# Performance work log

Hardware: AMD Instinct MI355X
Metric: run time of the kernel (lower is better)

## Reference

```python
import jax, jax.numpy as jnp
import numpy as np

B, H, W, DIM = 8, 32, 32, 768
NUM_HEADS = 12
HEAD_DIM = DIM // NUM_HEADS  # 64
SCALE = HEAD_DIM ** (-0.5)


def setup_inputs() -> dict:
    key = jax.random.key(0)
    ks = jax.random.split(key, 7)
    return {
        "x": jax.random.normal(ks[0], (B, H, W, DIM), dtype=jnp.float32),
        "qkv_w": jax.random.normal(ks[1], (DIM, 3 * DIM), dtype=jnp.float32) * 0.02,
        "qkv_b": jax.random.normal(ks[2], (3 * DIM,), dtype=jnp.float32) * 0.02,
        "proj_w": jax.random.normal(ks[3], (DIM, DIM), dtype=jnp.float32) * 0.02,
        "proj_b": jax.random.normal(ks[4], (DIM,), dtype=jnp.float32) * 0.02,
        "rel_pos_h": jax.random.normal(ks[5], (2 * H - 1, HEAD_DIM), dtype=jnp.float32) * 0.02,
        "rel_pos_w": jax.random.normal(ks[6], (2 * W - 1, HEAD_DIM), dtype=jnp.float32) * 0.02,
    }


def _get_rel_pos(q_size, k_size, rel_pos):
    # q_size == k_size here, so no interpolation branch; coords in [0, 2*size-2]
    coords = jnp.arange(q_size)[:, None] - jnp.arange(k_size)[None, :] + (k_size - 1)
    return rel_pos[coords]  # [q_size, k_size, head_dim]


def reference(x, qkv_w, qkv_b, proj_w, proj_b, rel_pos_h, rel_pos_w):
    b, h, w, dim = x.shape
    n = h * w
    qkv = x.reshape(b, n, dim) @ qkv_w + qkv_b                      # [B, N, 3*dim]
    qkv = qkv.reshape(b, n, 3, NUM_HEADS, HEAD_DIM)
    qkv = jnp.transpose(qkv, (2, 0, 3, 1, 4)).reshape(3, b * NUM_HEADS, n, HEAD_DIM)
    q, k, v = qkv[0], qkv[1], qkv[2]                                # [B*nh, N, hd]

    attn = jnp.einsum("bqc,bkc->bqk", q * SCALE, k)                 # [B*nh, N, N]

    Rh = _get_rel_pos(h, h, rel_pos_h)                              # [H, H, hd]
    Rw = _get_rel_pos(w, w, rel_pos_w)                              # [W, W, hd]
    r_q = q.reshape(b * NUM_HEADS, h, w, HEAD_DIM)
    rel_h = jnp.einsum("bhwc,hkc->bhwk", r_q, Rh)                   # [B*nh, H, W, H]
    rel_w = jnp.einsum("bhwc,wkc->bhwk", r_q, Rw)                   # [B*nh, H, W, W]
    attn = (attn.reshape(b * NUM_HEADS, h, w, h, w)
            + rel_h[:, :, :, :, None]
            + rel_w[:, :, :, None, :]).reshape(b * NUM_HEADS, n, n)

    attn = jax.nn.softmax(attn, axis=-1)
    out = jnp.einsum("bqk,bkc->bqc", attn, v)                       # [B*nh, N, hd]
    out = out.reshape(b, NUM_HEADS, h, w, HEAD_DIM)
    out = jnp.transpose(out, (0, 2, 3, 1, 4)).reshape(b, h, w, dim)
    return out @ proj_w + proj_b
```

## Files before the change

### kernel.cpp

```cpp
#include <hip/hip_runtime.h>


typedef __bf16 bf16;
typedef __bf16 bf16x8 __attribute__((ext_vector_type(8)));
typedef __bf16 bf16x4 __attribute__((ext_vector_type(4)));
typedef __bf16 bf16x2 __attribute__((ext_vector_type(2)));
typedef float f32x4 __attribute__((ext_vector_type(4)));
typedef unsigned int u32x2 __attribute__((ext_vector_type(2)));

#define MFMA16(a, b, c) __builtin_amdgcn_mfma_f32_16x16x32_bf16((a), (b), (c), 0, 0, 0)

__device__ __forceinline__ void gld_lds16(const void* g, void* l) {
  __builtin_amdgcn_global_load_lds(
      (const __attribute__((address_space(1))) void*)g,
      (__attribute__((address_space(3))) void*)l, 16, 0, 0);
}

__global__ __launch_bounds__(256) void prep_k(const float* __restrict__ x,
                                              const float* __restrict__ qkv_w,
                                              const float* __restrict__ proj_w,
                                              const float* __restrict__ rh,
                                              const float* __restrict__ rw,
                                              bf16* __restrict__ xb,
                                              bf16* __restrict__ WqkvT,
                                              bf16* __restrict__ WprojT,
                                              bf16* __restrict__ rhb,
                                              bf16* __restrict__ rwb) {
  __shared__ float tile[64][65];
  int b = blockIdx.x, tid = threadIdx.x;
  if (b >= 616) {
    int i = (b - 616) * 256 + tid;
    float4 a = ((const float4*)x)[i * 2];
    float4 c = ((const float4*)x)[i * 2 + 1];
    bf16x8 v;
    v[0] = (bf16)a.x; v[1] = (bf16)a.y; v[2] = (bf16)a.z; v[3] = (bf16)a.w;
    v[4] = (bf16)c.x; v[5] = (bf16)c.y; v[6] = (bf16)c.z; v[7] = (bf16)c.w;
    *(bf16x8*)(xb + (size_t)i * 8) = v;
    return;
  }
  if (b >= 576) {
    int idx = (b - 576) * 256 + tid;
    int tab = idx >= 5120;
    int local = idx - (tab ? 5120 : 0);
    int r = local >> 6, c = local & 63;
    const float* src = tab ? rw : rh;
    bf16* dst = tab ? rwb : rhb;
    dst[r * 64 + c] = (bf16)((r < 63) ? src[r * 64 + c] : 0.f);
    return;
  }
  const float* in; bf16* out; int N, k0, n0;
  if (b < 432) { in = qkv_w; out = WqkvT; N = 2304; k0 = (b % 12) * 64; n0 = (b / 12) * 64; }
  else { int bb = b - 432; in = proj_w; out = WprojT; N = 768; k0 = (bb % 12) * 64; n0 = (bb / 12) * 64; }
#pragma unroll
  for (int it = 0; it < 4; ++it) {
    int f4 = it * 256 + tid;
    int row = f4 >> 4, c4 = f4 & 15;
    float4 v = *(const float4*)(in + (size_t)(k0 + row) * N + n0 + c4 * 4);
    tile[row][c4 * 4 + 0] = v.x; tile[row][c4 * 4 + 1] = v.y;
    tile[row][c4 * 4 + 2] = v.z; tile[row][c4 * 4 + 3] = v.w;
  }
  __syncthreads();
#pragma unroll
  for (int it = 0; it < 2; ++it) {
    int f8 = it * 256 + tid;
    int nrow = f8 >> 3, kc = (f8 & 7) * 8;
    bf16x8 v;
#pragma unroll
    for (int i = 0; i < 8; ++i) v[i] = (bf16)tile[kc + i][nrow];
    *(bf16x8*)(out + (size_t)(n0 + nrow) * 768 + k0 + kc) = v;
  }
}

template <int MODE>
__global__ __launch_bounds__(256) void gemm_bt_k(const bf16* __restrict__ A,
                                                 const bf16* __restrict__ Bt,
                                                 const float* __restrict__ bias,
                                                 void* __restrict__ outp,
                                                 bf16* __restrict__ vt,
                                                 int M, int N, int K) {
  __shared__ bf16 lA[128 * 32];
  __shared__ bf16 lB[128 * 32];
  int tid = threadIdx.x;
  int wid = tid >> 6, lane = tid & 63;
  int lr = lane & 15, lg = lane >> 4;
  int m0 = blockIdx.x * 128, n0 = blockIdx.y * 128;
  int wr = (wid >> 1) * 64, wc = (wid & 1) * 64;

  const f32x4 fz = {0.f, 0.f, 0.f, 0.f};
  f32x4 acc[4][4];
#pragma unroll
  for (int i = 0; i < 4; ++i)
#pragma unroll
    for (int j = 0; j < 4; ++j) acc[i][j] = fz;

  for (int k0 = 0; k0 < K; k0 += 32) {
    __syncthreads();
#pragma unroll
    for (int it = 0; it < 2; ++it) {
      int e = it * 2048 + tid * 8;
      int row = e >> 5, col = e & 31;
      gld_lds16(A + (size_t)(m0 + row) * K + k0 + col, &lA[it * 2048 + wid * 512]);
      gld_lds16(Bt + (size_t)(n0 + row) * K + k0 + col, &lB[it * 2048 + wid * 512]);
    }
    __syncthreads();
    bf16x8 af[4], bfr[4];
#pragma unroll
    for (int i = 0; i < 4; ++i) {
      af[i]  = *(const bf16x8*)(&lA[(wr + i * 16 + lr) * 32 + lg * 8]);
      bfr[i] = *(const bf16x8*)(&lB[(wc + i * 16 + lr) * 32 + lg * 8]);
    }
#pragma unroll
    for (int mi = 0; mi < 4; ++mi)
#pragma unroll
      for (int ni = 0; ni < 4; ++ni)
        acc[mi][ni] = MFMA16(af[mi], bfr[ni], acc[mi][ni]);
  }

  if (MODE == 0) {
    bf16* qkv = (bf16*)outp;
#pragma unroll
    for (int ni = 0; ni < 4; ++ni) {
      int j = n0 + wc + ni * 16 + lr;
      int three = j / 768;
      int rem = j - three * 768;
      int head = rem >> 6, c = rem & 63;
      float bv = bias[j];
#pragma unroll
      for (int mi = 0; mi < 4; ++mi) {
        int mrow = m0 + wr + mi * 16 + lg * 4;
        int b_ = mrow >> 10, n = mrow & 1023;
        if (three == 2) {
          bf16x4 w4;
#pragma unroll
          for (int r = 0; r < 4; ++r) w4[r] = (bf16)(acc[mi][ni][r] + bv);
          *(bf16x4*)(vt + ((size_t)(b_ * 12 + head) << 16) + (size_t)c * 1024 + n) = w4;
        } else {
          bf16* p = qkv + (size_t)three * 6291456 +
                    ((size_t)(b_ * 12 + head) << 16) + ((size_t)n << 6) + c;
#pragma unroll
          for (int r = 0; r < 4; ++r)
            p[(size_t)r << 6] = (bf16)(acc[mi][ni][r] + bv);
        }
      }
    }
  } else {
    float* Co = (float*)outp;
#pragma unroll
    for (int ni = 0; ni < 4; ++ni) {
      int j = n0 + wc + ni * 16 + lr;
      float bv = bias[j];
#pragma unroll
      for (int mi = 0; mi < 4; ++mi) {
        int mrow = m0 + wr + mi * 16 + lg * 4;
        float* p = Co + (size_t)mrow * N + j;
#pragma unroll
        for (int r = 0; r < 4; ++r)
          p[(size_t)r * N] = acc[mi][ni][r] + bv;
      }
    }
  }
}

__global__ __launch_bounds__(256) void attn_k(const bf16* __restrict__ Qg,
                                              const bf16* __restrict__ Kg,
                                              const bf16* __restrict__ Vg,
                                              const bf16* __restrict__ RHb,
                                              const bf16* __restrict__ RWb,
                                              bf16* __restrict__ attout) {
  __shared__ __align__(16) char smem[40448];
  bf16* lK    = (bf16*)smem;
  bf16* lV    = (bf16*)(smem + 9216);
  bf16* relhd = (bf16*)(smem + 18432);
  unsigned int* lPw = (unsigned int*)(smem + 31232);

  int bid = blockIdx.x;
  int j8 = bid >> 3;
  int bh = (bid & 7) * 12 + (j8 >> 3);
  int qt = j8 & 7;
  int bb = bh / 12, head = bh - bb * 12;
  int tid = threadIdx.x, wid = tid >> 6, lane = tid & 63;
  int lr = lane & 15, lg = lane >> 4;
  const size_t bhoff = (size_t)bh << 16;
  const f32x4 fz = {0.f, 0.f, 0.f, 0.f};
  const float LOG2E = 1.44269504f;

  int srow = tid >> 3, scol = (tid & 7) * 8;
  const bf16* Ksrc = Kg + bhoff + (size_t)srow * 64 + scol;
  const bf16* Vsrc = Vg + bhoff + (size_t)srow * 1024 + scol;

  bf16x8 kr0 = *(const bf16x8*)(Ksrc);
  bf16x8 kr1 = *(const bf16x8*)(Ksrc + 32 * 64);
  bf16x8 vr0 = *(const bf16x8*)(Vsrc);
  bf16x8 vr1 = *(const bf16x8*)(Vsrc + 32 * 1024);

  bf16x8 qa[2][2];
#pragma unroll
  for (int f = 0; f < 2; ++f)
#pragma unroll
    for (int h = 0; h < 2; ++h)
      qa[f][h] = *(const bf16x8*)(Qg + bhoff +
                   (size_t)(qt * 128 + wid * 32 + f * 16 + lr) * 64 + h * 32 + lg * 8);

  bf16* scr = (bf16*)(smem + wid * 4352);
#pragma unroll
  for (int f = 0; f < 2; ++f)
#pragma unroll
    for (int tt = 0; tt < 4; ++tt) {
      bf16x8 w0 = *(const bf16x8*)(RWb + (tt * 16 + lr) * 64 + lg * 8);
      bf16x8 w1 = *(const bf16x8*)(RWb + (tt * 16 + lr) * 64 + 32 + lg * 8);
      f32x4 dw = MFMA16(w0, qa[f][0], fz);
      dw = MFMA16(w1, qa[f][1], dw);
#pragma unroll
      for (int r = 0; r < 4; ++r)
        scr[(f * 16 + lr) * 68 + tt * 16 + lg * 4 + r] = (bf16)dw[r];
    }
  float rws[2][8];
#pragma unroll
  for (int f = 0; f < 2; ++f)
#pragma unroll
    for (int tb = 0; tb < 2; ++tb)
#pragma unroll
      for (int r = 0; r < 4; ++r) {
        int kd = (f * 16 + lr) - (tb * 16 + lg * 4 + r) + 31;
        rws[f][tb * 4 + r] = LOG2E * (float)scr[(f * 16 + lr) * 68 + kd];
      }

#pragma unroll
  for (int f = 0; f < 2; ++f)
#pragma unroll
    for (int tt = 0; tt < 3; ++tt) {
      bf16x8 h0 = *(const bf16x8*)(RHb + (4 * qt + tt * 16 + lr) * 64 + lg * 8);
      bf16x8 h1 = *(const bf16x8*)(RHb + (4 * qt + tt * 16 + lr) * 64 + 32 + lg * 8);
      f32x4 dh = MFMA16(h0, qa[f][0], fz);
      dh = MFMA16(h1, qa[f][1], dh);
#pragma unroll
      for (int r = 0; r < 4; ++r)
        relhd[(wid * 32 + f * 16 + lr) * 50 + tt * 16 + lg * 4 + r] = (bf16)dh[r];
    }
  __syncthreads();

  f32x4 oacc[2][4], accl[2];
  bf16x8 ones;
#pragma unroll
  for (int i = 0; i < 8; ++i) ones[i] = (bf16)1.0f;
#pragma unroll
  for (int f = 0; f < 2; ++f) {
    accl[f] = fz;
#pragma unroll
    for (int ct = 0; ct < 4; ++ct) oacc[f][ct] = fz;
  }

  unsigned int* lPmy = lPw + wid * 576;

  for (int kb = 0; kb < 16; ++kb) {
    *(bf16x8*)(&lK[srow * 72 + scol]) = kr0;
    *(bf16x8*)(&lK[(srow + 32) * 72 + scol]) = kr1;
    *(bf16x8*)(&lV[srow * 72 + scol]) = vr0;
    *(bf16x8*)(&lV[(srow + 32) * 72 + scol]) = vr1;
    if (kb < 15) {
      const bf16* kp = Ksrc + (kb + 1) * 4096;
      const bf16* vp = Vsrc + (kb + 1) * 64;
      kr0 = *(const bf16x8*)(kp);
      kr1 = *(const bf16x8*)(kp + 32 * 64);
      vr0 = *(const bf16x8*)(vp);
      vr1 = *(const bf16x8*)(vp + 32 * 1024);
    }
    __syncthreads();

#pragma unroll
    for (int f = 0; f < 2; ++f) {
      f32x4 s[4];
      __builtin_amdgcn_s_setprio(1);
#pragma unroll
      for (int t = 0; t < 4; ++t) {
        bf16x8 kf0 = *(const bf16x8*)(&lK[(t * 16 + lr) * 72 + lg * 8]);
        bf16x8 kf1 = *(const bf16x8*)(&lK[(t * 16 + lr) * 72 + 32 + lg * 8]);
        s[t] = MFMA16(kf0, qa[f][0], fz);
        s[t] = MFMA16(kf1, qa[f][1], s[t]);
      }
      __builtin_amdgcn_s_setprio(0);
      int rowb = (wid * 32 + f * 16 + lr) * 50;
      float rh0 = LOG2E * (float)relhd[rowb + wid + 31 - 2 * kb];
      float rh1 = LOG2E * (float)relhd[rowb + wid + 30 - 2 * kb];

#pragma unroll
      for (int t = 0; t < 4; ++t)
#pragma unroll
        for (int r = 0; r < 4; ++r)
          s[t][r] = exp2f(fmaf(s[t][r], 0.18033688f,
                               (t < 2 ? rh0 : rh1) + rws[f][(t & 1) * 4 + r]));

#pragma unroll
      for (int t = 0; t < 4; ++t) {
        bf16x2 p0 = {(bf16)s[t][0], (bf16)s[t][1]};
        bf16x2 p1 = {(bf16)s[t][2], (bf16)s[t][3]};
        u32x2 w2 = {__builtin_bit_cast(unsigned int, p0),
                    __builtin_bit_cast(unsigned int, p1)};
        *(u32x2*)(&lPmy[lr * 36 + t * 8 + lg * 2]) = w2;
      }
      __builtin_amdgcn_s_setprio(1);
#pragma unroll
      for (int kk = 0; kk < 2; ++kk) {
        bf16x8 pf = *(const bf16x8*)(&lPmy[lr * 36 + kk * 16 + lg * 4]);
        accl[f] = MFMA16(ones, pf, accl[f]);
#pragma unroll
        for (int ct = 0; ct < 4; ++ct) {
          bf16x8 vf = *(const bf16x8*)(&lV[(ct * 16 + lr) * 72 + kk * 32 + lg * 8]);
          oacc[f][ct] = MFMA16(vf, pf, oacc[f][ct]);
        }
      }
      __builtin_amdgcn_s_setprio(0);
    }
    __syncthreads();
  }

#pragma unroll
  for (int f = 0; f < 2; ++f) {
    float rl = 1.f / accl[f][0];
    int n = qt * 128 + wid * 32 + f * 16 + lr;
#pragma unroll
    for (int ct = 0; ct < 4; ++ct) {
      bf16x4 w4;
#pragma unroll
      for (int r = 0; r < 4; ++r) w4[r] = (bf16)(oacc[f][ct][r] * rl);
      *(bf16x4*)(attout + (size_t)(bb * 1024 + n) * 768 + head * 64 + ct * 16 + lg * 4) = w4;
    }
  }
}

extern "C" void kernel_launch(void* const* d_in, const int* in_sizes, int n_in,
                              void* d_out, int out_size, void* d_ws, size_t ws_size,
                              hipStream_t stream) {
  const float* x      = (const float*)d_in[0];
  const float* qkv_w  = (const float*)d_in[1];
  const float* qkv_b  = (const float*)d_in[2];
  const float* proj_w = (const float*)d_in[3];
  const float* proj_b = (const float*)d_in[4];
  const float* relph  = (const float*)d_in[5];
  const float* relpw  = (const float*)d_in[6];
  float* out = (float*)d_out;

  char* ws = (char*)d_ws;
  size_t off = 0;
  auto alloc = [&](size_t bytes) -> void* {
    void* p = ws + off;
    off += (bytes + 255) & ~(size_t)255;
    return p;
  };
  bf16* xb     = (bf16*)alloc(8192UL * 768 * 2);
  bf16* WqkvT  = (bf16*)alloc(2304UL * 768 * 2);
  bf16* WprojT = (bf16*)alloc(768UL * 768 * 2);
  bf16* QKVb   = (bf16*)alloc(2UL * 96 * 1024 * 64 * 2);
  bf16* VTb    = (bf16*)alloc(96UL * 64 * 1024 * 2);
  bf16* RHb    = (bf16*)alloc(80UL * 64 * 2);
  bf16* RWb    = (bf16*)alloc(80UL * 64 * 2);
  bf16* attb   = xb;

  prep_k<<<dim3(3688), dim3(256), 0, stream>>>(x, qkv_w, proj_w, relph, relpw,
                                               xb, WqkvT, WprojT, RHb, RWb);
  gemm_bt_k<0><<<dim3(64, 18), dim3(256), 0, stream>>>(xb, WqkvT, qkv_b,
                                                       (void*)QKVb, VTb, 8192, 2304, 768);
  attn_k<<<dim3(768), dim3(256), 0, stream>>>(QKVb, QKVb + 6291456, VTb,
                                              RHb, RWb, attb);
  gemm_bt_k<1><<<dim3(64, 6), dim3(256), 0, stream>>>(attb, WprojT, proj_b,
                                                      (void*)out, nullptr, 8192, 768, 768);
}
```

Baseline: 220.3 us.

## Deepen GEMM K-tile to 64 with XOR-swizzled LDS and narrower proj tiles

The GEMM kernel now stages a 64-wide K slice per iteration instead of 32, which halves the number of barrier pairs. LDS columns are XOR-swizzled by row so the 16-byte fragment reads avoid bank conflicts. A BN template parameter lets the output projection use 64-column tiles, doubling its grid to 768 blocks for better CU occupancy. The cost is more LDS per block, and the narrower proj tiles reload A more often.

```diff
diff --git a/kernel.cpp b/kernel.cpp
--- a/kernel.cpp
+++ b/kernel.cpp
@@ -71,55 +71,66 @@
   }
 }
 
-template <int MODE>
+template <int MODE, int BN>
 __global__ __launch_bounds__(256) void gemm_bt_k(const bf16* __restrict__ A,
                                                  const bf16* __restrict__ Bt,
                                                  const float* __restrict__ bias,
                                                  void* __restrict__ outp,
                                                  bf16* __restrict__ vt,
                                                  int M, int N, int K) {
-  __shared__ bf16 lA[128 * 32];
-  __shared__ bf16 lB[128 * 32];
+  __shared__ bf16 lA[128 * 64];
+  __shared__ bf16 lB[BN * 64];
+  constexpr int NI = BN / 32;
   int tid = threadIdx.x;
   int wid = tid >> 6, lane = tid & 63;
   int lr = lane & 15, lg = lane >> 4;
-  int m0 = blockIdx.x * 128, n0 = blockIdx.y * 128;
-  int wr = (wid >> 1) * 64, wc = (wid & 1) * 64;
+  int m0 = blockIdx.x * 128, n0 = blockIdx.y * BN;
+  int wr = (wid >> 1) * 64, wc = (wid & 1) * (BN / 2);
 
   const f32x4 fz = {0.f, 0.f, 0.f, 0.f};
-  f32x4 acc[4][4];
+  f32x4 acc[4][NI];
 #pragma unroll
   for (int i = 0; i < 4; ++i)
 #pragma unroll
-    for (int j = 0; j < 4; ++j) acc[i][j] = fz;
-
-  for (int k0 = 0; k0 < K; k0 += 32) {
+    for (int j = 0; j < NI; ++j) acc[i][j] = fz;
+
+  int srow = tid >> 3;
+  int ug = (tid & 7) ^ (srow & 7);
+  int rs = lr & 7;
+
+  for (int k0 = 0; k0 < K; k0 += 64) {
     __syncthreads();
 #pragma unroll
-    for (int it = 0; it < 2; ++it) {
-      int e = it * 2048 + tid * 8;
-      int row = e >> 5, col = e & 31;
-      gld_lds16(A + (size_t)(m0 + row) * K + k0 + col, &lA[it * 2048 + wid * 512]);
-      gld_lds16(Bt + (size_t)(n0 + row) * K + k0 + col, &lB[it * 2048 + wid * 512]);
-    }
+    for (int it = 0; it < 4; ++it)
+      gld_lds16(A + (size_t)(m0 + it * 32 + srow) * K + k0 + ug * 8,
+                &lA[it * 2048 + wid * 512]);
+#pragma unroll
+    for (int it = 0; it < NI; ++it)
+      gld_lds16(Bt + (size_t)(n0 + it * 32 + srow) * K + k0 + ug * 8,
+                &lB[it * 2048 + wid * 512]);
     __syncthreads();
-    bf16x8 af[4], bfr[4];
-#pragma unroll
-    for (int i = 0; i < 4; ++i) {
-      af[i]  = *(const bf16x8*)(&lA[(wr + i * 16 + lr) * 32 + lg * 8]);
-      bfr[i] = *(const bf16x8*)(&lB[(wc + i * 16 + lr) * 32 + lg * 8]);
-    }
-#pragma unroll
-    for (int mi = 0; mi < 4; ++mi)
-#pragma unroll
-      for (int ni = 0; ni < 4; ++ni)
-        acc[mi][ni] = MFMA16(af[mi], bfr[ni], acc[mi][ni]);
+#pragma unroll
+    for (int h = 0; h < 2; ++h) {
+      bf16x8 af[4], bfr[NI];
+      int ul = ((h * 4 + lg) ^ rs) * 8;
+#pragma unroll
+      for (int i = 0; i < 4; ++i)
+        af[i] = *(const bf16x8*)(&lA[(wr + i * 16 + lr) * 64 + ul]);
+#pragma unroll
+      for (int i = 0; i < NI; ++i)
+        bfr[i] = *(const bf16x8*)(&lB[(wc + i * 16 + lr) * 64 + ul]);
+#pragma unroll
+      for (int mi = 0; mi < 4; ++mi)
+#pragma unroll
+        for (int ni = 0; ni < NI; ++ni)
+          acc[mi][ni] = MFMA16(af[mi], bfr[ni], acc[mi][ni]);
+    }
   }
 
   if (MODE == 0) {
     bf16* qkv = (bf16*)outp;
 #pragma unroll
-    for (int ni = 0; ni < 4; ++ni) {
+    for (int ni = 0; ni < NI; ++ni) {
       int j = n0 + wc + ni * 16 + lr;
       int three = j / 768;
       int rem = j - three * 768;
@@ -146,7 +157,7 @@
   } else {
     float* Co = (float*)outp;
 #pragma unroll
-    for (int ni = 0; ni < 4; ++ni) {
+    for (int ni = 0; ni < NI; ++ni) {
       int j = n0 + wc + ni * 16 + lr;
       float bv = bias[j];
 #pragma unroll
@@ -358,10 +369,10 @@
 
   prep_k<<<dim3(3688), dim3(256), 0, stream>>>(x, qkv_w, proj_w, relph, relpw,
                                                xb, WqkvT, WprojT, RHb, RWb);
-  gemm_bt_k<0><<<dim3(64, 18), dim3(256), 0, stream>>>(xb, WqkvT, qkv_b,
-                                                       (void*)QKVb, VTb, 8192, 2304, 768);
+  gemm_bt_k<0, 128><<<dim3(64, 18), dim3(256), 0, stream>>>(xb, WqkvT, qkv_b,
+                                                            (void*)QKVb, VTb, 8192, 2304, 768);
   attn_k<<<dim3(768), dim3(256), 0, stream>>>(QKVb, QKVb + 6291456, VTb,
                                               RHb, RWb, attb);
-  gemm_bt_k<1><<<dim3(64, 6), dim3(256), 0, stream>>>(attb, WprojT, proj_b,
-                                                      (void*)out, nullptr, 8192, 768, 768);
-}
+  gemm_bt_k<1, 64><<<dim3(64, 12), dim3(256), 0, stream>>>(attb, WprojT, proj_b,
+                                                           (void*)out, nullptr, 8192, 768, 768);
+}
```

Result: faster. 209.8 us (-4.8%).
